# Performance work log

Hardware: AMD Instinct MI355X
Metric: run time of the kernel (lower is better)

The kernel has to match this reference:

```python
import jax, jax.numpy as jnp
import numpy as np

N, L, S, H, D = 2, 2048, 2048, 8, 64

def elu_feature_map(x):
    return jax.nn.elu(x) + 1.0

def setup_inputs() -> dict:
    key = jax.random.key(0)
    k1, k2, k3, k4, k5 = jax.random.split(key, 5)
    return {
        "queries": jax.random.normal(k1, (N, L, H, D), dtype=jnp.float32),
        "keys": jax.random.normal(k2, (N, S, H, D), dtype=jnp.float32),
        "values": jax.random.normal(k3, (N, S, H, D), dtype=jnp.float32),
        "q_mask": jnp.ones((N, L), dtype=jnp.float32),
        "kv_mask": jnp.ones((N, S), dtype=jnp.float32),
        "W": jax.random.normal(k4, (1, 2), dtype=jnp.float32) * 0.5,  # nn.Linear(2,1) weight
        "b": jax.random.normal(k5, (1,), dtype=jnp.float32) * 0.5,    # nn.Linear(2,1) bias
    }

def reference(queries, keys, values, q_mask, kv_mask, W, b):
    # feature map: elu(x) + 1
    Q = elu_feature_map(queries) * q_mask[:, :, None, None]   # [N,L,H,D]
    K = elu_feature_map(keys) * kv_mask[:, :, None, None]     # [N,S,H,D]
    queries_m = queries * q_mask[:, :, None, None]
    values_m = values * kv_mask[:, :, None, None]  # masked but unused downstream (as in original)
    del values_m
    # full QK score tensor [N,L,S,H]
    qk = jnp.einsum('nlhd,nshd->nlsh', Q, K)
    qk_mean = jnp.mean(qk, axis=2)  # [N,L,H]
    qk_max = jnp.max(qk, axis=2)    # [N,L,H]
    stats = jnp.stack([qk_mean, qk_max], axis=-1)  # [N,L,H,2]
    gate = jax.nn.sigmoid(jnp.einsum('nlhe,oe->nlho', stats, W) + b)  # [N,L,H,1]
    atten = gate[..., 0]  # [N,L,H]
    return queries_m * atten[..., None]  # [N,L,H,D]
```

## Files before the change

kernel.cpp:

```cpp
#include <hip/hip_runtime.h>
#include <math.h>

#define N_ 2
#define L_ 2048
#define S_ 2048
#define H_ 8
#define D_ 64

#define BLK_L 256
#define BS 64
#define SSPLIT 4
#define KPAD 72

typedef __attribute__((ext_vector_type(8))) short short8;
typedef __attribute__((ext_vector_type(4))) float floatx4;

__device__ __forceinline__ float feat(float x) {
    return x > 0.0f ? x + 1.0f : __expf(x);
}
__device__ __forceinline__ short f2bf(float x) {
    unsigned u = __float_as_uint(x);
    unsigned r = (u + 0x7fffu + ((u >> 16) & 1u)) >> 16;
    return (short)r;
}
__device__ __forceinline__ float bf2f(short h) {
    return __uint_as_float(((unsigned)(unsigned short)h) << 16);
}

__global__ __launch_bounds__(256) void ksum_kernel(const float* __restrict__ K,
        const float* __restrict__ kvmask, float* __restrict__ Ksum) {
    int nh = blockIdx.x;
    int z = blockIdx.y;
    int n = nh >> 3, h = nh & 7;
    int t = threadIdx.x;
    int d = t & 63, sc = t >> 6;
    float sum = 0.f;
    int s0 = z * 64 + sc * 16;
    #pragma unroll
    for (int k = 0; k < 16; ++k) {
        int s = s0 + k;
        float v = K[(((size_t)n * S_ + s) * H_ + h) * D_ + d];
        sum += feat(v) * kvmask[n * S_ + s];
    }
    __shared__ float sm[256];
    sm[t] = sum;
    __syncthreads();
    if (t < 64) {
        float tot = sm[t] + sm[t + 64] + sm[t + 128] + sm[t + 192];
        atomicAdd(&Ksum[nh * 64 + t], tot);
    }
}

__global__ __launch_bounds__(256) void rowmax_mfma(
        const float* __restrict__ Q, const float* __restrict__ K,
        const float* __restrict__ qmask, const float* __restrict__ kvmask,
        float* __restrict__ rowmaxg) {
    __shared__ short Kh[BS * KPAD];
    __shared__ short Kl[BS * KPAD];

    int nh = blockIdx.y;
    int n = nh >> 3, h = nh & 7;
    int t = threadIdx.x;
    int w = t >> 6, lane = t & 63;
    int quad = lane >> 4, l16 = lane & 15;
    int lblock = blockIdx.x * BLK_L;
    int z = blockIdx.z;

    short8 Ah[4][2], Al[4][2];
    #pragma unroll
    for (int lsub = 0; lsub < 4; ++lsub) {
        int lrow = lblock + w * 64 + lsub * 16 + l16;
        float qm = qmask[n * L_ + lrow];
        const float* qp = Q + (((size_t)n * L_ + lrow) * H_ + h) * D_ + quad * 8;
        #pragma unroll
        for (int ks = 0; ks < 2; ++ks) {
            float4 v0 = *(const float4*)(qp + ks * 32);
            float4 v1 = *(const float4*)(qp + ks * 32 + 4);
            float fv[8];
            fv[0] = feat(v0.x) * qm; fv[1] = feat(v0.y) * qm;
            fv[2] = feat(v0.z) * qm; fv[3] = feat(v0.w) * qm;
            fv[4] = feat(v1.x) * qm; fv[5] = feat(v1.y) * qm;
            fv[6] = feat(v1.z) * qm; fv[7] = feat(v1.w) * qm;
            short8 hi, lo;
            #pragma unroll
            for (int j = 0; j < 8; ++j) {
                short hb = f2bf(fv[j]);
                hi[j] = hb;
                lo[j] = f2bf(fv[j] - bf2f(hb));
            }
            Ah[lsub][ks] = hi;
            Al[lsub][ks] = lo;
        }
    }

    float rmax[4][4];
    #pragma unroll
    for (int i = 0; i < 4; ++i)
        #pragma unroll
        for (int r = 0; r < 4; ++r) rmax[i][r] = 0.f;

    const int tiles = S_ / SSPLIT / BS;
    for (int tile = 0; tile < tiles; ++tile) {
        int sbase = z * (S_ / SSPLIT) + tile * BS;
        __syncthreads();
        {
            int row = t >> 2, chunk = t & 3;
            float km = kvmask[n * S_ + sbase + row];
            const float* kp = K + (((size_t)n * S_ + sbase + row) * H_ + h) * D_ + chunk * 16;
            float fv[16];
            #pragma unroll
            for (int j = 0; j < 4; ++j) {
                float4 v = *(const float4*)(kp + j * 4);
                fv[4 * j + 0] = feat(v.x) * km;
                fv[4 * j + 1] = feat(v.y) * km;
                fv[4 * j + 2] = feat(v.z) * km;
                fv[4 * j + 3] = feat(v.w) * km;
            }
            short8 h0, h1, l0, l1;
            #pragma unroll
            for (int j = 0; j < 8; ++j) {
                short hb = f2bf(fv[j]);
                h0[j] = hb;
                l0[j] = f2bf(fv[j] - bf2f(hb));
                short hb2 = f2bf(fv[8 + j]);
                h1[j] = hb2;
                l1[j] = f2bf(fv[8 + j] - bf2f(hb2));
            }
            short* dh = &Kh[row * KPAD + chunk * 16];
            short* dl = &Kl[row * KPAD + chunk * 16];
            *(short8*)(dh)     = h0;
            *(short8*)(dh + 8) = h1;
            *(short8*)(dl)     = l0;
            *(short8*)(dl + 8) = l1;
        }
        __syncthreads();

        #pragma unroll
        for (int ssub = 0; ssub < 4; ++ssub) {
            const short* bph = &Kh[(ssub * 16 + l16) * KPAD + quad * 8];
            const short* bpl = &Kl[(ssub * 16 + l16) * KPAD + quad * 8];
            short8 Bh0 = *(const short8*)(bph);
            short8 Bh1 = *(const short8*)(bph + 32);
            short8 Bl0 = *(const short8*)(bpl);
            short8 Bl1 = *(const short8*)(bpl + 32);
            #pragma unroll
            for (int lsub = 0; lsub < 4; ++lsub) {
                floatx4 acc = {0.f, 0.f, 0.f, 0.f};
                acc = __builtin_amdgcn_mfma_f32_16x16x32_bf16(Ah[lsub][0], Bh0, acc, 0, 0, 0);
                acc = __builtin_amdgcn_mfma_f32_16x16x32_bf16(Ah[lsub][1], Bh1, acc, 0, 0, 0);
                acc = __builtin_amdgcn_mfma_f32_16x16x32_bf16(Ah[lsub][0], Bl0, acc, 0, 0, 0);
                acc = __builtin_amdgcn_mfma_f32_16x16x32_bf16(Ah[lsub][1], Bl1, acc, 0, 0, 0);
                acc = __builtin_amdgcn_mfma_f32_16x16x32_bf16(Al[lsub][0], Bh0, acc, 0, 0, 0);
                acc = __builtin_amdgcn_mfma_f32_16x16x32_bf16(Al[lsub][1], Bh1, acc, 0, 0, 0);
                #pragma unroll
                for (int r = 0; r < 4; ++r)
                    rmax[lsub][r] = fmaxf(rmax[lsub][r], acc[r]);
            }
        }
    }

    #pragma unroll
    for (int lsub = 0; lsub < 4; ++lsub)
        #pragma unroll
        for (int r = 0; r < 4; ++r) {
            float m = rmax[lsub][r];
            m = fmaxf(m, __shfl_xor(m, 1, 64));
            m = fmaxf(m, __shfl_xor(m, 2, 64));
            m = fmaxf(m, __shfl_xor(m, 4, 64));
            m = fmaxf(m, __shfl_xor(m, 8, 64));
            if (l16 == 0) {
                int l = lblock + w * 64 + lsub * 16 + quad * 4 + r;
                atomicMax((unsigned*)&rowmaxg[(size_t)nh * L_ + l],
                          __float_as_uint(m));
            }
        }
}

__global__ __launch_bounds__(256) void finalize_kernel(
        const float* __restrict__ Q, const float* __restrict__ qmask,
        const float* __restrict__ Ksum, const float* __restrict__ rowmaxg,
        const float* __restrict__ W, const float* __restrict__ b,
        float* __restrict__ out) {
    int t = threadIdx.x;
    int lane = t & 63;
    int wid = (blockIdx.x << 2) | (t >> 6);
    int n = wid / (L_ * H_);
    int lh = wid % (L_ * H_);
    int l = lh / H_, h = lh % H_;

    float q = Q[(size_t)wid * 64 + lane];
    float qm = qmask[n * L_ + l];
    float p = feat(q) * qm * Ksum[(n * H_ + h) * 64 + lane];
    #pragma unroll
    for (int off = 32; off > 0; off >>= 1)
        p += __shfl_xor(p, off, 64);
    float mean = p * (1.0f / S_);
    float mx = rowmaxg[((size_t)n * H_ + h) * L_ + l];
    float zz = W[0] * mean + W[1] * mx + b[0];
    float g = 1.0f / (1.0f + __expf(-zz));
    out[(size_t)wid * 64 + lane] = q * qm * g;
}

extern "C" void kernel_launch(void* const* d_in, const int* in_sizes, int n_in,
                              void* d_out, int out_size, void* d_ws, size_t ws_size,
                              hipStream_t stream) {
    const float* Q      = (const float*)d_in[0];
    const float* K      = (const float*)d_in[1];
    const float* qmask  = (const float*)d_in[3];
    const float* kvmask = (const float*)d_in[4];
    const float* W      = (const float*)d_in[5];
    const float* b      = (const float*)d_in[6];
    float* out = (float*)d_out;

    float* Ksum   = (float*)d_ws;
    float* rowmax = (float*)d_ws + 1024;

    hipMemsetAsync(Ksum, 0, 1024 * sizeof(float), stream);
    hipMemsetAsync(rowmax, 0, (size_t)N_ * H_ * L_ * sizeof(float), stream);

    ksum_kernel<<<dim3(N_ * H_, 32), 256, 0, stream>>>(K, kvmask, Ksum);
    rowmax_mfma<<<dim3(L_ / BLK_L, N_ * H_, SSPLIT), 256, 0, stream>>>(
        Q, K, qmask, kvmask, rowmax);
    finalize_kernel<<<dim3(N_ * L_ * H_ / 4), 256, 0, stream>>>(
        Q, qmask, Ksum, rowmax, W, b, out);
}
```

Baseline: 123.5 us.

## Double-buffer K tiles in rowmax kernel and replace atomics with partial buffers

The rowmax kernel now prefetches the next K tile into registers while MFMAs run on the current LDS buffer, using two LDS buffers and one barrier per tile. Atomic accumulation of Ksum and the row max is replaced by per-split partial arrays that the finalize kernel reduces. This removes the two memset launches and atomic contention. Finalize is reorganized so each block handles 64 rows of one (n,h) and reduces the partials once per thread. The costs are twice the LDS, more registers for the prefetch, and extra reads of the partial arrays in finalize.

```diff
diff --git a/kernel.cpp b/kernel.cpp
--- a/kernel.cpp
+++ b/kernel.cpp
@@ -10,7 +10,9 @@
 #define BLK_L 256
 #define BS 64
 #define SSPLIT 4
+#define TILES (S_ / SSPLIT / BS)
 #define KPAD 72
+#define KP 16
 
 typedef __attribute__((ext_vector_type(8))) short short8;
 typedef __attribute__((ext_vector_type(4))) float floatx4;
@@ -28,16 +30,16 @@
 }
 
 __global__ __launch_bounds__(256) void ksum_kernel(const float* __restrict__ K,
-        const float* __restrict__ kvmask, float* __restrict__ Ksum) {
+        const float* __restrict__ kvmask, float* __restrict__ Kpart) {
     int nh = blockIdx.x;
     int z = blockIdx.y;
     int n = nh >> 3, h = nh & 7;
     int t = threadIdx.x;
     int d = t & 63, sc = t >> 6;
     float sum = 0.f;
-    int s0 = z * 64 + sc * 16;
-    #pragma unroll
-    for (int k = 0; k < 16; ++k) {
+    int s0 = z * (S_ / KP) + sc * 32;
+    #pragma unroll 4
+    for (int k = 0; k < 32; ++k) {
         int s = s0 + k;
         float v = K[(((size_t)n * S_ + s) * H_ + h) * D_ + d];
         sum += feat(v) * kvmask[n * S_ + s];
@@ -46,17 +48,17 @@
     sm[t] = sum;
     __syncthreads();
     if (t < 64) {
-        float tot = sm[t] + sm[t + 64] + sm[t + 128] + sm[t + 192];
-        atomicAdd(&Ksum[nh * 64 + t], tot);
+        Kpart[(z * 16 + nh) * 64 + t] =
+            sm[t] + sm[t + 64] + sm[t + 128] + sm[t + 192];
     }
 }
 
 __global__ __launch_bounds__(256) void rowmax_mfma(
         const float* __restrict__ Q, const float* __restrict__ K,
         const float* __restrict__ qmask, const float* __restrict__ kvmask,
-        float* __restrict__ rowmaxg) {
-    __shared__ short Kh[BS * KPAD];
-    __shared__ short Kl[BS * KPAD];
+        float* __restrict__ rowpart) {
+    __shared__ short Kh[2][BS * KPAD];
+    __shared__ short Kl[2][BS * KPAD];
 
     int nh = blockIdx.y;
     int n = nh >> 3, h = nh & 7;
@@ -93,52 +95,64 @@
         }
     }
 
+    int srow = t >> 2, chunk = t & 3;
+    float4 sv[4];
+    float skm;
+
+    auto loadreg = [&](int tile) {
+        int sbase = z * (S_ / SSPLIT) + tile * BS;
+        const float* kp = K + (((size_t)n * S_ + sbase + srow) * H_ + h) * D_ + chunk * 16;
+        sv[0] = *(const float4*)(kp);
+        sv[1] = *(const float4*)(kp + 4);
+        sv[2] = *(const float4*)(kp + 8);
+        sv[3] = *(const float4*)(kp + 12);
+        skm = kvmask[n * S_ + sbase + srow];
+    };
+    auto storelds = [&](int buf) {
+        float fv[16];
+        #pragma unroll
+        for (int j = 0; j < 4; ++j) {
+            fv[4 * j + 0] = feat(sv[j].x) * skm;
+            fv[4 * j + 1] = feat(sv[j].y) * skm;
+            fv[4 * j + 2] = feat(sv[j].z) * skm;
+            fv[4 * j + 3] = feat(sv[j].w) * skm;
+        }
+        short8 h0, h1, l0, l1;
+        #pragma unroll
+        for (int j = 0; j < 8; ++j) {
+            short hb = f2bf(fv[j]);
+            h0[j] = hb;
+            l0[j] = f2bf(fv[j] - bf2f(hb));
+            short hb2 = f2bf(fv[8 + j]);
+            h1[j] = hb2;
+            l1[j] = f2bf(fv[8 + j] - bf2f(hb2));
+        }
+        short* dh = &Kh[buf][srow * KPAD + chunk * 16];
+        short* dl = &Kl[buf][srow * KPAD + chunk * 16];
+        *(short8*)(dh)     = h0;
+        *(short8*)(dh + 8) = h1;
+        *(short8*)(dl)     = l0;
+        *(short8*)(dl + 8) = l1;
+    };
+
     float rmax[4][4];
     #pragma unroll
     for (int i = 0; i < 4; ++i)
         #pragma unroll
         for (int r = 0; r < 4; ++r) rmax[i][r] = 0.f;
 
-    const int tiles = S_ / SSPLIT / BS;
-    for (int tile = 0; tile < tiles; ++tile) {
-        int sbase = z * (S_ / SSPLIT) + tile * BS;
-        __syncthreads();
-        {
-            int row = t >> 2, chunk = t & 3;
-            float km = kvmask[n * S_ + sbase + row];
-            const float* kp = K + (((size_t)n * S_ + sbase + row) * H_ + h) * D_ + chunk * 16;
-            float fv[16];
-            #pragma unroll
-            for (int j = 0; j < 4; ++j) {
-                float4 v = *(const float4*)(kp + j * 4);
-                fv[4 * j + 0] = feat(v.x) * km;
-                fv[4 * j + 1] = feat(v.y) * km;
-                fv[4 * j + 2] = feat(v.z) * km;
-                fv[4 * j + 3] = feat(v.w) * km;
-            }
-            short8 h0, h1, l0, l1;
-            #pragma unroll
-            for (int j = 0; j < 8; ++j) {
-                short hb = f2bf(fv[j]);
-                h0[j] = hb;
-                l0[j] = f2bf(fv[j] - bf2f(hb));
-                short hb2 = f2bf(fv[8 + j]);
-                h1[j] = hb2;
-                l1[j] = f2bf(fv[8 + j] - bf2f(hb2));
-            }
-            short* dh = &Kh[row * KPAD + chunk * 16];
-            short* dl = &Kl[row * KPAD + chunk * 16];
-            *(short8*)(dh)     = h0;
-            *(short8*)(dh + 8) = h1;
-            *(short8*)(dl)     = l0;
-            *(short8*)(dl + 8) = l1;
-        }
-        __syncthreads();
+    loadreg(0);
+    storelds(0);
+    __syncthreads();
+
+    for (int tile = 0; tile < TILES; ++tile) {
+        int cur = tile & 1;
+        if (tile + 1 < TILES) loadreg(tile + 1);
 
         #pragma unroll
         for (int ssub = 0; ssub < 4; ++ssub) {
-            const short* bph = &Kh[(ssub * 16 + l16) * KPAD + quad * 8];
-            const short* bpl = &Kl[(ssub * 16 + l16) * KPAD + quad * 8];
+            const short* bph = &Kh[cur][(ssub * 16 + l16) * KPAD + quad * 8];
+            const short* bpl = &Kl[cur][(ssub * 16 + l16) * KPAD + quad * 8];
             short8 Bh0 = *(const short8*)(bph);
             short8 Bh1 = *(const short8*)(bph + 32);
             short8 Bl0 = *(const short8*)(bpl);
@@ -157,6 +171,9 @@
                     rmax[lsub][r] = fmaxf(rmax[lsub][r], acc[r]);
             }
         }
+
+        if (tile + 1 < TILES) storelds(1 - cur);
+        __syncthreads();
     }
 
     #pragma unroll
@@ -170,35 +187,45 @@
             m = fmaxf(m, __shfl_xor(m, 8, 64));
             if (l16 == 0) {
                 int l = lblock + w * 64 + lsub * 16 + quad * 4 + r;
-                atomicMax((unsigned*)&rowmaxg[(size_t)nh * L_ + l],
-                          __float_as_uint(m));
+                rowpart[((size_t)z * 16 + nh) * L_ + l] = m;
             }
         }
 }
 
 __global__ __launch_bounds__(256) void finalize_kernel(
         const float* __restrict__ Q, const float* __restrict__ qmask,
-        const float* __restrict__ Ksum, const float* __restrict__ rowmaxg,
+        const float* __restrict__ Kpart, const float* __restrict__ rowpart,
         const float* __restrict__ W, const float* __restrict__ b,
         float* __restrict__ out) {
+    int nh = blockIdx.y;
+    int n = nh >> 3, h = nh & 7;
+    int lblock = blockIdx.x * 64;
     int t = threadIdx.x;
-    int lane = t & 63;
-    int wid = (blockIdx.x << 2) | (t >> 6);
-    int n = wid / (L_ * H_);
-    int lh = wid % (L_ * H_);
-    int l = lh / H_, h = lh % H_;
-
-    float q = Q[(size_t)wid * 64 + lane];
-    float qm = qmask[n * L_ + l];
-    float p = feat(q) * qm * Ksum[(n * H_ + h) * 64 + lane];
-    #pragma unroll
-    for (int off = 32; off > 0; off >>= 1)
-        p += __shfl_xor(p, off, 64);
-    float mean = p * (1.0f / S_);
-    float mx = rowmaxg[((size_t)n * H_ + h) * L_ + l];
-    float zz = W[0] * mean + W[1] * mx + b[0];
-    float g = 1.0f / (1.0f + __expf(-zz));
-    out[(size_t)wid * 64 + lane] = q * qm * g;
+    int w = t >> 6, lane = t & 63;
+
+    float ks = 0.f;
+    #pragma unroll
+    for (int p = 0; p < KP; ++p)
+        ks += Kpart[(p * 16 + nh) * 64 + lane];
+
+    float w0 = W[0], w1 = W[1], bb = b[0];
+
+    #pragma unroll 4
+    for (int r = 0; r < 16; ++r) {
+        int l = lblock + w * 16 + r;
+        float q = Q[(((size_t)n * L_ + l) * H_ + h) * D_ + lane];
+        float qm = qmask[n * L_ + l];
+        float p = feat(q) * qm * ks;
+        #pragma unroll
+        for (int off = 32; off > 0; off >>= 1)
+            p += __shfl_xor(p, off, 64);
+        float mx = 0.f;
+        #pragma unroll
+        for (int zz = 0; zz < SSPLIT; ++zz)
+            mx = fmaxf(mx, rowpart[((size_t)zz * 16 + nh) * L_ + l]);
+        float g = 1.0f / (1.0f + __expf(-(w0 * p * (1.0f / S_) + w1 * mx + bb)));
+        out[(((size_t)n * L_ + l) * H_ + h) * D_ + lane] = q * qm * g;
+    }
 }
 
 extern "C" void kernel_launch(void* const* d_in, const int* in_sizes, int n_in,
@@ -212,15 +239,12 @@
     const float* b      = (const float*)d_in[6];
     float* out = (float*)d_out;
 
-    float* Ksum   = (float*)d_ws;
-    float* rowmax = (float*)d_ws + 1024;
-
-    hipMemsetAsync(Ksum, 0, 1024 * sizeof(float), stream);
-    hipMemsetAsync(rowmax, 0, (size_t)N_ * H_ * L_ * sizeof(float), stream);
-
-    ksum_kernel<<<dim3(N_ * H_, 32), 256, 0, stream>>>(K, kvmask, Ksum);
+    float* Kpart   = (float*)d_ws;
+    float* rowpart = (float*)d_ws + KP * 16 * 64;
+
+    ksum_kernel<<<dim3(N_ * H_, KP), 256, 0, stream>>>(K, kvmask, Kpart);
     rowmax_mfma<<<dim3(L_ / BLK_L, N_ * H_, SSPLIT), 256, 0, stream>>>(
-        Q, K, qmask, kvmask, rowmax);
-    finalize_kernel<<<dim3(N_ * L_ * H_ / 4), 256, 0, stream>>>(
-        Q, qmask, Ksum, rowmax, W, b, out);
-}
+        Q, K, qmask, kvmask, rowpart);
+    finalize_kernel<<<dim3(L_ / 64, N_ * H_), 256, 0, stream>>>(
+        Q, qmask, Kpart, rowpart, W, b, out);
+}
```

Result: slower. 132.3 us (+7.2%).
